# Kernel tuning notes

Hardware: AMD Instinct MI355X
Metric: run time of the kernel (lower is better)

## Reference

```python
import jax, jax.numpy as jnp
import numpy as np

HEAD_DIM = 128
N_HEADS = 32
ROPE_DIM = 64
TOPK = 1024
B, S, HID, QLORA = 1, 2048, 4096, 1536
LN_EPS = 1e-5  # torch nn.LayerNorm default


def _hadamard_matrix(n):
    H = np.array([[1.0]], dtype=np.float32)
    while H.shape[0] < n:
        H = np.block([[H, H], [H, -H]])
    return jnp.asarray(H)

_H128 = _hadamard_matrix(HEAD_DIM)
_FWHT_SCALE = HEAD_DIM ** -0.5


def rotate_activation(x):
    # Fast Walsh-Hadamard transform == x @ H_sylvester, scaled by dim**-0.5
    return (x @ _H128) * _FWHT_SCALE


def rope_non_interleaved(x, cos, sin):
    # x: [..., rope_dim]; cos/sin: broadcastable [..., rope_dim/2]
    half = x.shape[-1] // 2
    x1, x2 = x[..., :half], x[..., half:]
    return jnp.concatenate([x1 * cos - x2 * sin, x1 * sin + x2 * cos], axis=-1)


def setup_inputs() -> dict:
    key = jax.random.key(0)
    ks = jax.random.split(key, 8)
    hidden_states = jax.random.normal(ks[0], (B, S, HID), jnp.float32)
    q_compressed = jax.random.normal(ks[1], (B, S, QLORA), jnp.float32)
    # rotary cos/sin for rope_dim=64 (standard concat layout)
    pos = jnp.arange(S, dtype=jnp.float32)
    inv_freq = 1.0 / (10000.0 ** (jnp.arange(0, ROPE_DIM, 2, dtype=jnp.float32) / ROPE_DIM))
    ang = pos[:, None] * inv_freq[None, :]  # [S, 32]
    cos = jnp.tile(jnp.cos(ang), (1, 2))[None]  # [1, S, 64]
    sin = jnp.tile(jnp.sin(ang), (1, 2))[None]
    # additive causal mask [B, S, S]
    causal = jnp.tril(jnp.ones((S, S), jnp.bool_))
    attention_mask = jnp.where(causal, 0.0, -1e9).astype(jnp.float32)[None]
    Wq_b = jax.random.normal(ks[2], (QLORA, N_HEADS * HEAD_DIM), jnp.float32) * (QLORA ** -0.5)
    Wk = jax.random.normal(ks[3], (HID, HEAD_DIM), jnp.float32) * (HID ** -0.5)
    k_gamma = jnp.ones((HEAD_DIM,), jnp.float32)
    k_beta = jnp.zeros((HEAD_DIM,), jnp.float32)
    Ww = jax.random.normal(ks[4], (HID, N_HEADS), jnp.float32) * (HID ** -0.5)
    return {"hidden_states": hidden_states, "q_compressed": q_compressed, "cos": cos,
            "sin": sin, "attention_mask": attention_mask, "Wq_b": Wq_b, "Wk": Wk,
            "k_gamma": k_gamma, "k_beta": k_beta, "Ww": Ww}


def reference(hidden_states, q_compressed, cos, sin, attention_mask, Wq_b, Wk, k_gamma, k_beta, Ww):
    b, s, _ = hidden_states.shape
    softmax_scale = HEAD_DIM ** -0.5
    # queries: [b, s, H, D]
    q = (q_compressed @ Wq_b).reshape(b, s, N_HEADS, HEAD_DIM)
    q_rope, q_nope = q[..., :ROPE_DIM], q[..., ROPE_DIM:]
    # keys: single shared head, LayerNorm(k)
    k = hidden_states @ Wk  # [b, s, D]
    mu = jnp.mean(k, axis=-1, keepdims=True)
    var = jnp.mean(jnp.square(k - mu), axis=-1, keepdims=True)
    k = (k - mu) * jax.lax.rsqrt(var + LN_EPS) * k_gamma + k_beta
    k_rope, k_nope = k[..., :ROPE_DIM], k[..., ROPE_DIM:]
    # non-interleaved RoPE (cos/sin truncated to half_dim=32)
    half = ROPE_DIM // 2
    c, sn = cos[..., :half], sin[..., :half]
    q_rope = rope_non_interleaved(q_rope, c[:, :, None, :], sn[:, :, None, :])
    k_rope = rope_non_interleaved(k_rope, c, sn)
    q = jnp.concatenate([q_rope, q_nope], axis=-1)
    k = jnp.concatenate([k_rope, k_nope], axis=-1)
    # Hadamard activation rotation
    q = rotate_activation(q)
    k = rotate_activation(k)
    # I_{t,s} = sum_h w_{t,h} * ReLU(q_{t,h} . k_s) * scale
    scores = jax.nn.relu(jnp.einsum('bthd,bsd->bths', q, k)) * softmax_scale
    weights = hidden_states @ Ww  # [b, t, H]
    index_scores = jnp.einsum('bths,bth->bts', scores, weights)
    index_scores = index_scores + attention_mask
    topk = min(TOPK, s)
    _, topk_indices = jax.lax.top_k(index_scores, topk)  # [b, s, topk]
    return topk_indices, index_scores
```

## Files before the change

### kernel.cpp

```cpp
#include <hip/hip_runtime.h>
#include <stdint.h>

#define S_LEN 2048
#define HID 4096
#define QLORA 1536
#define NH 32
#define HD 128
#define TOPK_N 1024
#define NEG_INF -1000000000.0f
#define INV_SQRT_HD 0.08838834764831844f

typedef __attribute__((ext_vector_type(8))) short short8;
typedef __attribute__((ext_vector_type(4))) short short4_;
typedef __attribute__((ext_vector_type(4))) float float4_;
typedef __attribute__((ext_vector_type(4))) unsigned uint4_;
typedef __attribute__((ext_vector_type(4))) int int4_;
typedef __attribute__((ext_vector_type(2))) int int2_;

__device__ __forceinline__ short f2bf(float x) {
  union { float f; unsigned u; } v; v.f = x;
  unsigned r = v.u + 0x7FFFu + ((v.u >> 16) & 1u);
  return (short)(r >> 16);
}

__device__ __forceinline__ unsigned f2ord(float x) {
  union { float f; unsigned u; } v; v.f = x;
  return v.u ^ (0x80000000u | (unsigned)((int)v.u >> 31));
}

__device__ __forceinline__ char f2fp8(float x) {
  return (char)__builtin_amdgcn_cvt_pk_fp8_f32(x, x, 0, 0);
}

__device__ __forceinline__ void gload_lds16(const void* g, void* l) {
  __builtin_amdgcn_global_load_lds((const __attribute__((address_space(1))) unsigned int*)g,
                                   (__attribute__((address_space(3))) unsigned int*)l, 16, 0, 0);
}

__device__ __forceinline__ int chswz(int c) { return c ^ ((c >> 3) & 7); }

__global__ __launch_bounds__(256) void prep_kernel(
    const float* __restrict__ hidden, short* __restrict__ hidb,
    const float* __restrict__ qc, char* __restrict__ qc8,
    float* __restrict__ kacc,
    const float* __restrict__ wqb, char* __restrict__ wq8T,
    const float* __restrict__ wk, const float* __restrict__ ww,
    short* __restrict__ kwT) {
  __shared__ __align__(8) char stile[4352];
  int bid = blockIdx.x;
  const int tid = threadIdx.x;
  if (bid < 8192) {
    int i = bid * 256 + tid;
    float4 v = ((const float4*)hidden)[i];
    short4_ o;
    o[0] = f2bf(v.x); o[1] = f2bf(v.y); o[2] = f2bf(v.z); o[3] = f2bf(v.w);
    ((short4_*)hidb)[i] = o;
    return;
  }
  if (bid < 9728) {
    int i = (bid - 8192) * 256 + tid;
    float4 f0 = ((const float4*)qc)[i * 2];
    float4 f1 = ((const float4*)qc)[i * 2 + 1];
    int lo = 0, hi = 0;
    lo = __builtin_amdgcn_cvt_pk_fp8_f32(f0.x, f0.y, lo, 0);
    lo = __builtin_amdgcn_cvt_pk_fp8_f32(f0.z, f0.w, lo, 1);
    hi = __builtin_amdgcn_cvt_pk_fp8_f32(f1.x, f1.y, hi, 0);
    hi = __builtin_amdgcn_cvt_pk_fp8_f32(f1.z, f1.w, hi, 1);
    ((int2_*)qc8)[i] = (int2_){lo, hi};
    return;
  }
  if (bid < 10048) {
    int i = (bid - 9728) * 256 + tid;
    ((float4_*)kacc)[i] = (float4_){0.f, 0.f, 0.f, 0.f};
    return;
  }
  if (bid < 13120) {
    char (*t8)[33] = (char(*)[33])stile;
    int b = bid - 10048;
    int k0 = (b >> 7) * 64, n0 = (b & 127) * 32;
    #pragma unroll
    for (int i = 0; i < 8; i++) {
      int e = tid + i * 256;
      int r = e >> 5, c = e & 31;
      float x = wqb[(size_t)(k0 + r) * HID + n0 + c];
      t8[r][c] = f2fp8(x);
    }
    __syncthreads();
    int nl = tid >> 3, jk = (tid & 7) * 8;
    union { char c[8]; long l; } o;
    #pragma unroll
    for (int j = 0; j < 8; j++) o.c[j] = t8[jk + j][nl];
    *(long*)(wq8T + (size_t)(n0 + nl) * QLORA + k0 + jk) = o.l;
    return;
  }
  short (*tile)[33] = (short(*)[33])stile;
  const float* in; short* out; int R, C, bx, by;
  if (bid < 13632) {
    int b2 = bid - 13120;
    in = wk; out = kwT; R = HID; C = HD; bx = b2 & 3; by = b2 >> 2;
  } else {
    int b3 = bid - 13632;
    in = ww; out = kwT + 128 * HID; R = HID; C = NH; bx = 0; by = b3;
  }
  int c0 = bx * 32, r0 = by * 32;
  int tx = tid & 31, ty = tid >> 5;
  #pragma unroll
  for (int i = 0; i < 32; i += 8)
    tile[ty + i][tx] = f2bf(in[(size_t)(r0 + ty + i) * C + c0 + tx]);
  __syncthreads();
  #pragma unroll
  for (int i = 0; i < 32; i += 8)
    out[(size_t)(c0 + ty + i) * R + r0 + tx] = tile[tx][ty + i];
}

#define QSTAGE8(kt, Ad, Bd) do { \
  _Pragma("unroll") \
  for (int i = 0; i < 4; i++) { \
    int m = w * 32 + i * 8 + lr; \
    int gb = (kt) * 128 + ((lc ^ (m & 7)) << 4); \
    gload_lds16(qc8 + (size_t)(t0 + m) * QLORA + gb, (Ad) + (w * 32 + i * 8) * 128); \
    gload_lds16(wq8T + (size_t)(n0 + m) * QLORA + gb, (Bd) + (w * 32 + i * 8) * 128); \
  } \
} while (0)

#define QCOMPUTE8(Aq, Bq) do { \
  _Pragma("unroll") \
  for (int p = 0; p < 4; p++) { \
    int ch = p * 2 + (quad >> 1); \
    int lo8 = (quad & 1) * 8; \
    long a[2], b[8]; \
    _Pragma("unroll") \
    for (int mt = 0; mt < 2; mt++) { \
      int m = w * 32 + mt * 16 + l15; \
      a[mt] = *(const long*)((Aq) + m * 128 + ((ch ^ (m & 7)) << 4) + lo8); \
    } \
    _Pragma("unroll") \
    for (int nt = 0; nt < 8; nt++) { \
      int n = nt * 16 + l15; \
      b[nt] = *(const long*)((Bq) + n * 128 + ((ch ^ (n & 7)) << 4) + lo8); \
    } \
    _Pragma("unroll") \
    for (int mt = 0; mt < 2; mt++) \
      _Pragma("unroll") \
      for (int nt = 0; nt < 8; nt++) \
        acc[mt][nt] = __builtin_amdgcn_mfma_f32_16x16x32_fp8_fp8(a[mt], b[nt], acc[mt][nt], 0, 0, 0); \
  } \
} while (0)

__global__ __launch_bounds__(256, 2) void gemms_kernel(
    const char* __restrict__ qc8, const char* __restrict__ wq8T,
    const float* __restrict__ cosp, const float* __restrict__ sinp,
    char* __restrict__ qrot8,
    const short* __restrict__ hidb, const short* __restrict__ kwT,
    float* __restrict__ kacc) {
  __shared__ __align__(16) char smem[65536];
  const int tid = threadIdx.x;
  const int w = tid >> 6, lane = tid & 63;
  const int l15 = lane & 15, quad = lane >> 4;
  const int lr = lane >> 3, lc = lane & 7;

  if (blockIdx.x >= 256) {
    char* A0 = smem;
    char* B0 = smem + 16384;
    char* A1 = smem + 32768;
    char* B1 = smem + 49152;
    const int bq = blockIdx.x - 256;
    const int n0 = (bq & 31) * 128;
    const int t0 = (bq >> 5) * 128;

    float4_ acc[2][8];
    #pragma unroll
    for (int mt = 0; mt < 2; mt++)
      #pragma unroll
      for (int i = 0; i < 8; i++) acc[mt][i] = (float4_){0.f, 0.f, 0.f, 0.f};

    QSTAGE8(0, A0, B0);
    __syncthreads();
    for (int kt = 0; kt < 12; kt += 2) {
      QSTAGE8(kt + 1, A1, B1);
      QCOMPUTE8(A0, B0);
      __syncthreads();
      if (kt + 2 < 12) QSTAGE8(kt + 2, A0, B0);
      QCOMPUTE8(A1, B1);
      __syncthreads();
    }

    #pragma unroll
    for (int mt = 0; mt < 2; mt++) {
      #pragma unroll
      for (int r = 0; r < 4; r++) {
        const int trow = t0 + w * 32 + mt * 16 + quad * 4 + r;
        float v[8];
        #pragma unroll
        for (int nt = 0; nt < 8; nt++) v[nt] = acc[mt][nt][r];
        float cc0 = cosp[trow * 64 + l15], cc1 = cosp[trow * 64 + 16 + l15];
        float ss0 = sinp[trow * 64 + l15], ss1 = sinp[trow * 64 + 16 + l15];
        float r0 = v[0] * cc0 - v[2] * ss0, r1 = v[1] * cc1 - v[3] * ss1;
        float r2 = v[0] * ss0 + v[2] * cc0, r3 = v[1] * ss1 + v[3] * cc1;
        v[0] = r0; v[1] = r1; v[2] = r2; v[3] = r3;
        char* orow = qrot8 + (size_t)trow * HID + n0;
        #pragma unroll
        for (int nt = 0; nt < 8; nt++)
          orow[nt * 16 + l15] = f2fp8(v[nt]);
      }
    }
  } else {
    short* Al = (short*)smem;
    short* Bl = (short*)(smem + 8192);
    const int b2 = blockIdx.x;
    const int kc0 = (b2 & 7) * 512;
    const int m0g = (b2 >> 3) * 64;

    float4_ acc[10];
    #pragma unroll
    for (int i = 0; i < 10; i++) acc[i] = (float4_){0.f, 0.f, 0.f, 0.f};

    for (int k0 = kc0; k0 < kc0 + 512; k0 += 64) {
      #pragma unroll
      for (int i = 0; i < 2; i++) {
        int m = w * 16 + i * 8 + lr;
        int gk = k0 + ((lc ^ (m & 7)) << 3);
        gload_lds16(hidb + (size_t)(m0g + m) * HID + gk, Al + (w * 16 + i * 8) * 64);
      }
      #pragma unroll
      for (int i = 0; i < 5; i++) {
        int n = w * 40 + i * 8 + lr;
        int gk = k0 + ((lc ^ (n & 7)) << 3);
        gload_lds16(kwT + (size_t)n * HID + gk, Bl + (w * 40 + i * 8) * 64);
      }
      __syncthreads();
      #pragma unroll
      for (int kk = 0; kk < 64; kk += 32) {
        int ca = (kk >> 3) + quad;
        int ma = w * 16 + l15;
        short8 a = *(const short8*)(Al + ma * 64 + ((ca ^ (ma & 7)) << 3));
        #pragma unroll
        for (int nt = 0; nt < 10; nt++) {
          int n = nt * 16 + l15;
          short8 b = *(const short8*)(Bl + n * 64 + ((ca ^ (n & 7)) << 3));
          acc[nt] = __builtin_amdgcn_mfma_f32_16x16x32_bf16(a, b, acc[nt], 0, 0, 0);
        }
      }
      __syncthreads();
    }
    #pragma unroll
    for (int nt = 0; nt < 10; nt++)
      #pragma unroll
      for (int r = 0; r < 4; r++) {
        int row = m0g + w * 16 + quad * 4 + r;
        atomicAdd(&kacc[(size_t)row * 160 + nt * 16 + l15], acc[nt][r]);
      }
  }
}

__global__ __launch_bounds__(256) void ln_rope_kernel(
    const float* __restrict__ kacc, const float* __restrict__ gamma,
    const float* __restrict__ beta, const float* __restrict__ cosp,
    const float* __restrict__ sinp, char* __restrict__ krot8) {
  const int tid = threadIdx.x;
  const int row = blockIdx.x * 16 + (tid >> 4);
  const int l16 = tid & 15;
  const int c0 = l16 * 8;
  const float* rp = kacc + (size_t)row * 160 + c0;
  float4 f0 = ((const float4*)rp)[0], f1 = ((const float4*)rp)[1];
  float v[8] = {f0.x, f0.y, f0.z, f0.w, f1.x, f1.y, f1.z, f1.w};
  float s = 0.f, ss = 0.f;
  #pragma unroll
  for (int j = 0; j < 8; j++) { s += v[j]; ss += v[j] * v[j]; }
  #pragma unroll
  for (int d = 1; d <= 8; d <<= 1) {
    s += __shfl_xor(s, d, 64); ss += __shfl_xor(ss, d, 64);
  }
  float mu = s * (1.0f / 128.0f);
  float var = ss * (1.0f / 128.0f) - mu * mu;
  float rs = rsqrtf(var + 1e-5f);
  #pragma unroll
  for (int j = 0; j < 8; j++)
    v[j] = (v[j] - mu) * rs * gamma[c0 + j] + beta[c0 + j];
  #pragma unroll
  for (int j = 0; j < 8; j++) {
    float p = __shfl_xor(v[j], 4, 64);
    if (l16 < 8) {
      int idx = (c0 + j) & 31;
      float c = cosp[row * 64 + idx], sn = sinp[row * 64 + idx];
      v[j] = v[j] * c + p * ((l16 < 4) ? -sn : sn);
    }
  }
  int lo = 0, hi = 0;
  lo = __builtin_amdgcn_cvt_pk_fp8_f32(v[0], v[1], lo, 0);
  lo = __builtin_amdgcn_cvt_pk_fp8_f32(v[2], v[3], lo, 1);
  hi = __builtin_amdgcn_cvt_pk_fp8_f32(v[4], v[5], hi, 0);
  hi = __builtin_amdgcn_cvt_pk_fp8_f32(v[6], v[7], hi, 1);
  *(int2_*)(krot8 + (size_t)row * 128 + c0) = (int2_){lo, hi};
}

__global__ __launch_bounds__(256, 3) void scores_kernel(
    const char* __restrict__ qrot8, const char* __restrict__ krot8,
    const float* __restrict__ kacc, float* __restrict__ isc) {
  __shared__ __align__(16) char smem[32768];
  char* buf0 = smem;
  char* buf1 = smem + 16384;

  const int tid = threadIdx.x;
  const int w = tid >> 6, lane = tid & 63;
  const int l15 = lane & 15, quad = lane >> 4;
  const int wm = w >> 1, wn = w & 1;
  const int lr8 = lane >> 3, lc8 = lane & 7;

  const int bid = blockIdx.x;
  const int strip = (bid < 256) ? bid : (767 - bid);
  const int t0 = strip * 4;
  const int nsb = (t0 + 3) / 128 + 1;

  const char* Abase = qrot8 + (size_t)t0 * 32 * 128;
  #pragma unroll
  for (int i = 0; i < 4; i++) {
    int m = i * 32 + w * 8 + lr8;
    int gofs = m * 128 + ((lc8 ^ (m & 7)) << 4);
    gload_lds16(Abase + gofs, buf0 + (i * 32 + w * 8) * 128);
    gload_lds16(krot8 + gofs, buf1 + (i * 32 + w * 8) * 128);
  }
  __syncthreads();

  long af[4][4];
  #pragma unroll
  for (int k4 = 0; k4 < 4; k4++) {
    int ch = k4 * 2 + (quad >> 1);
    int lo8 = (quad & 1) * 8;
    #pragma unroll
    for (int mt = 0; mt < 4; mt++) {
      int m = wm * 64 + mt * 16 + l15;
      af[k4][mt] = *(const long*)(buf0 + m * 128 + ((ch ^ (m & 7)) << 4) + lo8);
    }
  }

  const int t_a = t0 + wm * 2, t_b = t_a + 1;
  float wq[4][4];
  #pragma unroll
  for (int mt = 0; mt < 4; mt++) {
    int tt = (mt < 2) ? t_a : t_b;
    #pragma unroll
    for (int r = 0; r < 4; r++)
      wq[mt][r] = kacc[(size_t)tt * 160 + 128 + (mt & 1) * 16 + quad * 4 + r];
  }
  __syncthreads();

  for (int sb = 0; sb < nsb; sb++) {
    char* cur = (sb & 1) ? buf0 : buf1;
    if (sb + 1 < nsb) {
      char* nxt = (sb & 1) ? buf1 : buf0;
      const char* Bbase = krot8 + (size_t)(sb + 1) * 128 * 128;
      #pragma unroll
      for (int i = 0; i < 4; i++) {
        int m = i * 32 + w * 8 + lr8;
        int gofs = m * 128 + ((lc8 ^ (m & 7)) << 4);
        gload_lds16(Bbase + gofs, nxt + (i * 32 + w * 8) * 128);
      }
    }

    float4_ acc[4][4];
    #pragma unroll
    for (int mt = 0; mt < 4; mt++)
      #pragma unroll
      for (int nt = 0; nt < 4; nt++) acc[mt][nt] = (float4_){0.f, 0.f, 0.f, 0.f};

    #pragma unroll
    for (int k4 = 0; k4 < 4; k4++) {
      int ch = k4 * 2 + (quad >> 1);
      int lo8 = (quad & 1) * 8;
      long b[4];
      #pragma unroll
      for (int nt = 0; nt < 4; nt++) {
        int n = wn * 64 + nt * 16 + l15;
        b[nt] = *(const long*)(cur + n * 128 + ((ch ^ (n & 7)) << 4) + lo8);
      }
      #pragma unroll
      for (int mt = 0; mt < 4; mt++)
        #pragma unroll
        for (int nt = 0; nt < 4; nt++)
          acc[mt][nt] = __builtin_amdgcn_mfma_f32_16x16x32_fp8_fp8(af[k4][mt], b[nt], acc[mt][nt], 0, 0, 0);
    }

    #pragma unroll
    for (int nt = 0; nt < 4; nt++) {
      float pa = 0.f, pb = 0.f;
      #pragma unroll
      for (int r = 0; r < 4; r++) {
        pa += fmaxf(acc[0][nt][r], 0.f) * wq[0][r] + fmaxf(acc[1][nt][r], 0.f) * wq[1][r];
        pb += fmaxf(acc[2][nt][r], 0.f) * wq[2][r] + fmaxf(acc[3][nt][r], 0.f) * wq[3][r];
      }
      pa += __shfl_xor(pa, 16, 64); pa += __shfl_xor(pa, 32, 64);
      pb += __shfl_xor(pb, 16, 64); pb += __shfl_xor(pb, 32, 64);
      int s = sb * 128 + wn * 64 + nt * 16 + l15;
      if (quad == 0)
        isc[(size_t)t_a * S_LEN + s] = (s <= t_a) ? pa * INV_SQRT_HD : NEG_INF;
      else if (quad == 1)
        isc[(size_t)t_b * S_LEN + s] = (s <= t_b) ? pb * INV_SQRT_HD : NEG_INF;
    }

    __syncthreads();
  }

  if (wn == 0) {
    const int myrow = (lane < 32) ? t_a : t_b;
    const int l32 = lane & 31;
    float4_ nf = (float4_){NEG_INF, NEG_INF, NEG_INF, NEG_INF};
    float4_* rowp = (float4_*)(isc + (size_t)myrow * S_LEN);
    for (int i = nsb * 32 + l32; i < 512; i += 32) rowp[i] = nf;
  }
}

#define CEK(x, y, d) { if ((d) ? (v[x] < v[y]) : (v[x] > v[y])) { unsigned _t = v[x]; v[x] = v[y]; v[y] = _t; } }

__device__ __forceinline__ void shfl_phase(unsigned v[8], int j, int base, bool d) {
  const int delta = j >> 3;
  const bool keep_max = (((base & j) == 0) == d);
  #pragma unroll
  for (int r = 0; r < 8; r++) {
    unsigned pv = (unsigned)__shfl_xor((int)v[r], delta, 64);
    unsigned mx = v[r] > pv ? v[r] : pv;
    unsigned mn = v[r] > pv ? pv : v[r];
    v[r] = keep_max ? mx : mn;
  }
}

__device__ __forceinline__ void reg_phase(unsigned v[8], bool d) {
  CEK(0, 4, d); CEK(1, 5, d); CEK(2, 6, d); CEK(3, 7, d);
  CEK(0, 2, d); CEK(1, 3, d); CEK(4, 6, d); CEK(5, 7, d);
  CEK(0, 1, d); CEK(2, 3, d); CEK(4, 5, d); CEK(6, 7, d);
}

__device__ __forceinline__ void lds_phase(unsigned v[8], unsigned* keys, int tid, int base,
                                          int j, bool d) {
  const int c0 = tid * 2, c1 = c0 + 1;
  ((uint4_*)keys)[chswz(c0)] = (uint4_){v[0], v[1], v[2], v[3]};
  ((uint4_*)keys)[chswz(c1)] = (uint4_){v[4], v[5], v[6], v[7]};
  __syncthreads();
  const int ptid = tid ^ (j >> 3);
  uint4_ u0 = ((uint4_*)keys)[chswz(ptid * 2)];
  uint4_ u1 = ((uint4_*)keys)[chswz(ptid * 2 + 1)];
  unsigned p[8] = {u0[0], u0[1], u0[2], u0[3], u1[0], u1[1], u1[2], u1[3]};
  const bool keep_max = (((base & j) == 0) == d);
  #pragma unroll
  for (int r = 0; r < 8; r++) {
    unsigned mx = v[r] > p[r] ? v[r] : p[r];
    unsigned mn = v[r] > p[r] ? p[r] : v[r];
    v[r] = keep_max ? mx : mn;
  }
  __syncthreads();
}

__global__ __launch_bounds__(256) void topk_kernel(const float* __restrict__ isc,
                                                   int* __restrict__ idx_out) {
  __shared__ __align__(16) unsigned keys[2048];
  const int t = blockIdx.x;
  const int tid = threadIdx.x;
  const int base = tid * 8;
  unsigned v[8];
  {
    const float* row = isc + (size_t)t * S_LEN;
    float4 f0 = ((const float4*)row)[tid * 2];
    float4 f1 = ((const float4*)row)[tid * 2 + 1];
    v[0] = (f2ord(f0.x) & 0xFFFFF800u) | (unsigned)(2047 - base - 0);
    v[1] = (f2ord(f0.y) & 0xFFFFF800u) | (unsigned)(2047 - base - 1);
    v[2] = (f2ord(f0.z) & 0xFFFFF800u) | (unsigned)(2047 - base - 2);
    v[3] = (f2ord(f0.w) & 0xFFFFF800u) | (unsigned)(2047 - base - 3);
    v[4] = (f2ord(f1.x) & 0xFFFFF800u) | (unsigned)(2047 - base - 4);
    v[5] = (f2ord(f1.y) & 0xFFFFF800u) | (unsigned)(2047 - base - 5);
    v[6] = (f2ord(f1.z) & 0xFFFFF800u) | (unsigned)(2047 - base - 6);
    v[7] = (f2ord(f1.w) & 0xFFFFF800u) | (unsigned)(2047 - base - 7);
  }
  CEK(0, 1, true); CEK(2, 3, false); CEK(4, 5, true); CEK(6, 7, false);
  CEK(0, 2, true); CEK(1, 3, true); CEK(4, 6, false); CEK(5, 7, false);
  CEK(0, 1, true); CEK(2, 3, true); CEK(4, 5, false); CEK(6, 7, false);
  {
    bool d8 = ((base & 8) == 0);
    CEK(0, 4, d8); CEK(1, 5, d8); CEK(2, 6, d8); CEK(3, 7, d8);
    CEK(0, 2, d8); CEK(1, 3, d8); CEK(4, 6, d8); CEK(5, 7, d8);
    CEK(0, 1, d8); CEK(2, 3, d8); CEK(4, 5, d8); CEK(6, 7, d8);
  }
  #pragma unroll
  for (int kb = 4; kb <= 11; kb++) {
    const int k = 1 << kb;
    const bool d = ((base & k) == 0);
    for (int j = k >> 1; j >= 512; j >>= 1)
      lds_phase(v, keys, tid, base, j, d);
    {
      int jtop = (k >> 1) < 256 ? (k >> 1) : 256;
      for (int j = jtop; j >= 8; j >>= 1)
        shfl_phase(v, j, base, d);
    }
    reg_phase(v, d);
  }
  if (tid < 128) {
    int4_ o0, o1;
    #pragma unroll
    for (int r = 0; r < 4; r++) o0[r] = 2047 - (int)(v[r] & 0x7FFu);
    #pragma unroll
    for (int r = 0; r < 4; r++) o1[r] = 2047 - (int)(v[4 + r] & 0x7FFu);
    ((int4_*)(idx_out + (size_t)t * TOPK_N))[tid * 2] = o0;
    ((int4_*)(idx_out + (size_t)t * TOPK_N))[tid * 2 + 1] = o1;
  }
}

extern "C" void kernel_launch(void* const* d_in, const int* in_sizes, int n_in,
                              void* d_out, int out_size, void* d_ws, size_t ws_size,
                              hipStream_t stream) {
  const float* hidden = (const float*)d_in[0];
  const float* qc     = (const float*)d_in[1];
  const float* cosp   = (const float*)d_in[2];
  const float* sinp   = (const float*)d_in[3];
  const float* wqb    = (const float*)d_in[5];
  const float* wk     = (const float*)d_in[6];
  const float* gamma  = (const float*)d_in[7];
  const float* beta   = (const float*)d_in[8];
  const float* ww     = (const float*)d_in[9];

  char* ws = (char*)d_ws;
  short* hidb  = (short*)ws;
  char*  qc8   = (char*)(ws + 16777216);
  char*  wq8T  = (char*)(ws + 19922944);
  short* kwT   = (short*)(ws + 26214400);
  char*  krot8 = (char*)(ws + 27525120);
  char*  qrot8 = (char*)(ws + 27787264);
  float* kacc  = (float*)(ws + 36175872);

  int*   idx_out = (int*)d_out;
  float* isc     = ((float*)d_out) + (size_t)S_LEN * TOPK_N;

  prep_kernel<<<dim3(13760), dim3(256), 0, stream>>>(hidden, hidb, qc, qc8, kacc,
                                                     wqb, wq8T, wk, ww, kwT);
  gemms_kernel<<<dim3(768), dim3(256), 0, stream>>>(qc8, wq8T, cosp, sinp, qrot8,
                                                    hidb, kwT, kacc);
  ln_rope_kernel<<<dim3(128), dim3(256), 0, stream>>>(kacc, gamma, beta, cosp, sinp, krot8);
  scores_kernel<<<dim3(512), dim3(256), 0, stream>>>(qrot8, krot8, kacc, isc);
  topk_kernel<<<dim3(2048), dim3(256), 0, stream>>>(isc, idx_out);
}
```

Measured before the change: 248.2 us.

## Sort first half of topk rows with one wavefront per row using shuffles

Rows 0-1023 of the top-k sort are now handled by a single 64-lane wavefront per row, holding 16 keys per lane in registers. Cross-lane bitonic stages use shuffle-xor instead of shared memory and block barriers. Remaining rows keep the original block-per-row shared-memory bitonic sort, and the grid shrinks from 2048 to 1280 blocks. The aim is to cut barrier and LDS traffic, and the split is probably chosen because causal masking makes early rows cheap. The cost is higher register pressure from 16 keys per thread.

```diff
diff --git a/kernel.cpp b/kernel.cpp
--- a/kernel.cpp
+++ b/kernel.cpp
@@ -450,11 +450,74 @@
   __syncthreads();
 }
 
+#define CEW(x, y, dir) { if ((dir) ? (v[x] < v[y]) : (v[x] > v[y])) { unsigned _t = v[x]; v[x] = v[y]; v[y] = _t; } }
+
+__device__ __forceinline__ void reg_tail16(unsigned v[16], bool dir) {
+  #pragma unroll
+  for (int j = 8; j >= 1; j >>= 1)
+    #pragma unroll
+    for (int r = 0; r < 16; r++)
+      if ((r & j) == 0) CEW(r, r | j, dir);
+}
+
 __global__ __launch_bounds__(256) void topk_kernel(const float* __restrict__ isc,
                                                    int* __restrict__ idx_out) {
+  const int tid = threadIdx.x;
+  if (blockIdx.x < 256) {
+    const int w = tid >> 6, lane = tid & 63;
+    const int t = blockIdx.x * 4 + w;
+    const float* row = isc + (size_t)t * S_LEN;
+    unsigned v[16];
+    #pragma unroll
+    for (int i = 0; i < 4; i++) {
+      float4 f = ((const float4*)row)[lane * 4 + i];
+      unsigned e = (unsigned)(2047 - lane * 16 - i * 4);
+      v[i * 4 + 0] = (f2ord(f.x) & 0xFFFFF800u) | (e - 0);
+      v[i * 4 + 1] = (f2ord(f.y) & 0xFFFFF800u) | (e - 1);
+      v[i * 4 + 2] = (f2ord(f.z) & 0xFFFFF800u) | (e - 2);
+      v[i * 4 + 3] = (f2ord(f.w) & 0xFFFFF800u) | (e - 3);
+    }
+    #pragma unroll
+    for (int kb = 1; kb <= 3; kb++) {
+      const int k = 1 << kb;
+      #pragma unroll
+      for (int j = k >> 1; j >= 1; j >>= 1)
+        #pragma unroll
+        for (int r = 0; r < 16; r++)
+          if ((r & j) == 0) { const bool dir = ((r & k) == 0); CEW(r, r | j, dir); }
+    }
+    { const bool dir = ((lane & 1) == 0); reg_tail16(v, dir); }
+    #pragma unroll
+    for (int kb = 5; kb <= 10; kb++) {
+      const int k = 1 << kb;
+      const bool dir = ((lane & (k >> 4)) == 0);
+      #pragma unroll
+      for (int j = k >> 1; j >= 16; j >>= 1) {
+        const int delta = j >> 4;
+        const bool keep_max = (((lane & delta) == 0) == dir);
+        #pragma unroll
+        for (int r = 0; r < 16; r++) {
+          unsigned p = (unsigned)__shfl_xor((int)v[r], delta, 64);
+          unsigned mx = v[r] > p ? v[r] : p;
+          unsigned mn = v[r] > p ? p : v[r];
+          v[r] = keep_max ? mx : mn;
+        }
+      }
+      reg_tail16(v, dir);
+    }
+    int* orow = idx_out + (size_t)t * TOPK_N + lane * 16;
+    #pragma unroll
+    for (int i = 0; i < 4; i++) {
+      int4_ o;
+      #pragma unroll
+      for (int q = 0; q < 4; q++) o[q] = 2047 - (int)(v[i * 4 + q] & 0x7FFu);
+      ((int4_*)orow)[i] = o;
+    }
+    return;
+  }
+
   __shared__ __align__(16) unsigned keys[2048];
-  const int t = blockIdx.x;
-  const int tid = threadIdx.x;
+  const int t = 1024 + (blockIdx.x - 256);
   const int base = tid * 8;
   unsigned v[8];
   {
@@ -534,5 +597,5 @@
                                                     hidb, kwT, kacc);
   ln_rope_kernel<<<dim3(128), dim3(256), 0, stream>>>(kacc, gamma, beta, cosp, sinp, krot8);
   scores_kernel<<<dim3(512), dim3(256), 0, stream>>>(qrot8, krot8, kacc, isc);
-  topk_kernel<<<dim3(2048), dim3(256), 0, stream>>>(isc, idx_out);
-}
+  topk_kernel<<<dim3(1280), dim3(256), 0, stream>>>(isc, idx_out);
+}
```

New measurement: 275.6 us. +11.0%, slower.
